# Kernel optimization log

Hardware: AMD Instinct MI355X
Metric: run time of the kernel (lower is better)

## Reference

```python
import jax, jax.numpy as jnp
import numpy as np

B, T, C = 2, 192, 512
H, D = 8, 64  # num_heads, head_dim; inner_dim = H*D = C


def setup_inputs() -> dict:
    key = jax.random.key(0)
    k1, k2, k3 = jax.random.split(key, 3)
    x = jax.random.normal(k1, (B, T, C), dtype=jnp.float32)
    W_in = jax.random.normal(k2, (C, 5 * H * D), dtype=jnp.float32) * 0.02
    b_in = jnp.zeros((5 * H * D,), dtype=jnp.float32)
    W_out = jax.random.normal(k3, (H * D, C), dtype=jnp.float32) * 0.02
    b_out = jnp.zeros((C,), dtype=jnp.float32)
    return {"x": x, "W_in": W_in, "b_in": b_in, "W_out": W_out, "b_out": b_out}


def _split_heads(t):
    # (B,T,H*D) -> (B,H,T,D)
    return t.reshape(B, T, H, D).transpose(0, 2, 1, 3)


def reference(x, W_in, b_in, W_out, b_out):
    scale = D ** -0.5
    proj = x @ W_in + b_in  # (B,T,5*H*D)
    q, k1, v1, k2, v2 = jnp.split(proj, 5, axis=-1)
    q = _split_heads(q) * scale
    k1 = _split_heads(k1)
    v1 = _split_heads(v1)
    k2 = _split_heads(k2)
    v2 = _split_heads(v2)
    # trilinear logits: <q_i, k1_j, k2_k> / sqrt(D), computed in fp32
    logits = jnp.einsum('bhid,bhjd,bhkd->bhijk', q, k1, k2,
                        preferred_element_type=jnp.float32)
    # softmax over the joint (j,k) axes
    attn = jax.nn.softmax(logits.reshape(B, H, T, T * T), axis=-1)
    attn = attn.reshape(B, H, T, T, T).astype(x.dtype)
    # out_i[d] = sum_{j,k} attn[i,j,k] * v1_j[d] * v2_k[d]
    out = jnp.einsum('bhijk,bhjd,bhkd->bhid', attn, v1, v2)
    y = out.transpose(0, 2, 1, 3).reshape(B, T, H * D)  # merge heads
    return y @ W_out + b_out
```

## Files before the change

kernel.cpp:

```cpp
#include <hip/hip_runtime.h>


typedef float  v4f __attribute__((ext_vector_type(4)));
typedef short  v8s __attribute__((ext_vector_type(8)));

__device__ __forceinline__ unsigned short f2bf(float f) {
  unsigned u = __float_as_uint(f);
  u += 0x7fffu + ((u >> 16) & 1u);
  return (unsigned short)(u >> 16);
}
__device__ __forceinline__ float bf2f(unsigned short b) {
  return __uint_as_float(((unsigned)b) << 16);
}

#if __has_builtin(__builtin_amdgcn_exp2f)
#define EXP2F(x) __builtin_amdgcn_exp2f(x)
#else
#define EXP2F(x) exp2f(x)
#endif

#define MFMA32(a, b, c) __builtin_amdgcn_mfma_f32_16x16x32_bf16((a), (b), (c), 0, 0, 0)

#define QSCALE 0.18033688011112042f


__global__ __launch_bounds__(256) void proj_kernel(
    const float* __restrict__ x, const float* __restrict__ Win,
    const float* __restrict__ bin, float* __restrict__ wsf,
    unsigned short* __restrict__ wsh) {
  __shared__ float xs[8 * 512];
  __shared__ float red[8 * 128];
  const int tid = threadIdx.x;
  const int r0 = blockIdx.x * 8;
  const int jj = tid & 127, half = tid >> 7;
  const int j = blockIdx.y * 128 + jj;

  const float4* xsrc = (const float4*)(x + r0 * 512);
  float4* xdst = (float4*)xs;
  for (int idx = tid; idx < 1024; idx += 256) xdst[idx] = xsrc[idx];
  __syncthreads();

  float acc[8];
#pragma unroll
  for (int r = 0; r < 8; ++r) acc[r] = 0.f;
  const float* wp = Win + (half * 256) * 2560 + j;
  const float* xp = xs + half * 256;
#pragma unroll 4
  for (int k = 0; k < 256; ++k) {
    const float w = wp[k * 2560];
#pragma unroll
    for (int r = 0; r < 8; ++r) acc[r] = fmaf(xp[r * 512 + k], w, acc[r]);
  }
  if (half) {
#pragma unroll
    for (int r = 0; r < 8; ++r) red[r * 128 + jj] = acc[r];
  }
  __syncthreads();
  if (!half) {
    const float bv = bin[j];
    const int which = j >> 9, cc = j & 511, h = cc >> 6, d = cc & 63;
#pragma unroll
    for (int r = 0; r < 8; ++r) {
      const int m = r0 + r;
      const int b = (m >= 192) ? 1 : 0;
      const int t = m - (b ? 192 : 0);
      const int bh = b * 8 + h;
      const float val = acc[r] + red[r * 128 + jj] + bv;
      const int rm = ((bh * 192 + t) << 6) + d;
      if (which == 0)      wsf[rm] = val * QSCALE;
      else if (which == 1) wsh[rm] = f2bf(val);
      else if (which == 2) wsh[393216 + ((bh << 6) + d) * 192 + t] = f2bf(val);
      else if (which == 3) wsh[196608 + rm] = f2bf(val);
      else                 wsf[196608 + rm] = val;
    }
  }
}

__global__ __launch_bounds__(256, 2) void attn_kernel(
    const float* __restrict__ wsf, const unsigned short* __restrict__ wsh,
    float* __restrict__ accp, float* __restrict__ Sp) {
  __shared__ unsigned short smem[64 * 200 + 4 * 16 * 40];
  unsigned short* V1s = smem;

  const int tid  = threadIdx.x;
  const int wv   = tid >> 6;
  const int lane = tid & 63;
  const int c    = lane & 15;
  const int quad = lane >> 4;

  const int bb = blockIdx.x;
  const int kb = bb & 3;
  const int it = (bb >> 2) % 12;
  const int bh = bb / 48;

  const unsigned short* k1g = wsh + bh * 192 * 64;
  const unsigned short* v1g = wsh + 393216 + bh * 64 * 192;
  const unsigned short* k2g = wsh + 196608 + bh * 192 * 64;
  const float*          v2g = wsf + 196608 + bh * 192 * 64;

  for (int idx = tid; idx < 1536; idx += 256) {
    const int r = idx / 24, c8 = (idx % 24) * 8;
    *(uint4*)(V1s + r * 200 + c8) = *(const uint4*)(v1g + r * 192 + c8);
  }

  v8s k1f[12][2];
#pragma unroll
  for (int jt = 0; jt < 12; ++jt) {
    const unsigned short* kp = k1g + ((jt * 16 + c) << 6) + (quad << 3);
    k1f[jt][0] = *(const v8s*)(kp);
    k1f[jt][1] = *(const v8s*)(kp + 32);
  }

  const float* qg = wsf + ((bh * 192 + it * 16 + c) << 6) + (quad << 3);
  float q0[8], q1[8];
  {
    v4f qa = *(const v4f*)(qg), qb = *(const v4f*)(qg + 4);
    v4f qc = *(const v4f*)(qg + 32), qd = *(const v4f*)(qg + 36);
#pragma unroll
    for (int e = 0; e < 4; ++e) {
      q0[e] = qa[e]; q0[4 + e] = qb[e];
      q1[e] = qc[e]; q1[4 + e] = qd[e];
    }
  }
  __syncthreads();

  unsigned short* Pch = smem + 12800 + wv * 640;
  const v4f z = {0.f, 0.f, 0.f, 0.f};
  v4f acc0 = z, acc1 = z, acc2 = z, acc3 = z;
  float S0 = 0.f, S1 = 0.f, S2 = 0.f, S3 = 0.f;

  const int kstart = kb * 48 + wv * 12;
  for (int s = 0; s < 12; ++s) {
    const int k = kstart + s;
    const unsigned short* k2r = k2g + (k << 6) + (quad << 3);
    union { uint4 u4; unsigned short us[8]; } kl, kh;
    kl.u4 = *(const uint4*)k2r;
    kh.u4 = *(const uint4*)(k2r + 32);
    const float* v2r = v2g + (k << 6) + c;
    const float v20 = v2r[0], v21 = v2r[16], v22 = v2r[32], v23 = v2r[48];

    union { v8s v; unsigned short us[8]; } af0, af1;
#pragma unroll
    for (int e = 0; e < 8; ++e) {
      af0.us[e] = f2bf(q0[e] * bf2f(kl.us[e]));
      af1.us[e] = f2bf(q1[e] * bf2f(kh.us[e]));
    }

    v4f o0 = z, o1 = z, o2 = z, o3 = z;
#pragma unroll
    for (int jp = 0; jp < 6; ++jp) {
#pragma unroll
      for (int jj2 = 0; jj2 < 2; ++jj2) {
        const int jt = jp * 2 + jj2;
        v4f Cf = MFMA32(af0.v, k1f[jt][0], z);
        Cf = MFMA32(af1.v, k1f[jt][1], Cf);
        unsigned short* wp2 = Pch + (quad << 2) * 40 + jj2 * 16 + c;
        const float p0 = EXP2F(Cf[0]), p1 = EXP2F(Cf[1]);
        const float p2 = EXP2F(Cf[2]), p3 = EXP2F(Cf[3]);
        S0 += p0; S1 += p1; S2 += p2; S3 += p3;
        wp2[0]   = (unsigned short)(__float_as_uint(p0) >> 16);
        wp2[40]  = (unsigned short)(__float_as_uint(p1) >> 16);
        wp2[80]  = (unsigned short)(__float_as_uint(p2) >> 16);
        wp2[120] = (unsigned short)(__float_as_uint(p3) >> 16);
      }
      const v8s ap = *(const v8s*)(Pch + c * 40 + (quad << 3));
      const int vcol = jp * 32 + (quad << 3);
      o0 = MFMA32(ap, *(const v8s*)(V1s + (c)      * 200 + vcol), o0);
      o1 = MFMA32(ap, *(const v8s*)(V1s + (c + 16) * 200 + vcol), o1);
      o2 = MFMA32(ap, *(const v8s*)(V1s + (c + 32) * 200 + vcol), o2);
      o3 = MFMA32(ap, *(const v8s*)(V1s + (c + 48) * 200 + vcol), o3);
    }
    acc0 += o0 * v20; acc1 += o1 * v21; acc2 += o2 * v22; acc3 += o3 * v23;
  }

  __syncthreads();
  float* redA = (float*)smem;
  float* redS = (float*)smem + 4096;

#pragma unroll
  for (int m2 = 1; m2 < 16; m2 <<= 1) {
    S0 += __shfl_xor(S0, m2, 16);
    S1 += __shfl_xor(S1, m2, 16);
    S2 += __shfl_xor(S2, m2, 16);
    S3 += __shfl_xor(S3, m2, 16);
  }
  if (c == 0) {
    float* rs = redS + wv * 16 + (quad << 2);
    rs[0] = S0; rs[1] = S1; rs[2] = S2; rs[3] = S3;
  }
#pragma unroll
  for (int r = 0; r < 4; ++r) {
    float* rr = redA + wv * 1024 + (((quad << 2) + r) << 6) + c;
    rr[0] = acc0[r]; rr[16] = acc1[r]; rr[32] = acc2[r]; rr[48] = acc3[r];
  }
  __syncthreads();

  const int pbase = (bh * 12 + it) * 4 + kb;
  float* ap_out = accp + pbase * 1024;
  for (int idx = tid; idx < 1024; idx += 256)
    ap_out[idx] = redA[idx] + redA[1024 + idx] + redA[2048 + idx] + redA[3072 + idx];
  if (tid < 16)
    Sp[pbase * 16 + tid] = redS[tid] + redS[16 + tid] + redS[32 + tid] + redS[48 + tid];
}

__global__ __launch_bounds__(256) void outp_kernel(
    const float* __restrict__ accp, const float* __restrict__ Sp,
    const float* __restrict__ Wout, const float* __restrict__ bout,
    float* __restrict__ y) {
  __shared__ float as[4 * 512];
  __shared__ float red[4 * 128];
  const int tid = threadIdx.x;
  const int r0 = blockIdx.x * 4;
  for (int idx = tid; idx < 2048; idx += 256) {
    const int r = idx >> 9, cc = idx & 511;
    const int m = r0 + r;
    const int b = (m >= 192) ? 1 : 0;
    const int t = m - (b ? 192 : 0);
    const int h = cc >> 6, d = cc & 63;
    const int bh = b * 8 + h, itl = t >> 4, i = t & 15;
    const int pb = (bh * 12 + itl) * 4;
    float a = 0.f, Sv = 0.f;
#pragma unroll
    for (int s2 = 0; s2 < 4; ++s2) {
      a  += accp[(pb + s2) * 1024 + (i << 6) + d];
      Sv += Sp[(pb + s2) * 16 + i];
    }
    as[idx] = a / Sv;
  }
  __syncthreads();

  const int jj = tid & 127, half = tid >> 7;
  const int j = blockIdx.y * 128 + jj;
  float acc[4];
#pragma unroll
  for (int r = 0; r < 4; ++r) acc[r] = 0.f;
  const float* wp = Wout + (half * 256) * 512 + j;
  const float* xp = as + half * 256;
#pragma unroll 4
  for (int k = 0; k < 256; ++k) {
    const float w = wp[k * 512];
#pragma unroll
    for (int r = 0; r < 4; ++r) acc[r] = fmaf(xp[r * 512 + k], w, acc[r]);
  }
  if (half) {
#pragma unroll
    for (int r = 0; r < 4; ++r) red[r * 128 + jj] = acc[r];
  }
  __syncthreads();
  if (!half) {
    const float bv = bout[j];
#pragma unroll
    for (int r = 0; r < 4; ++r)
      y[(r0 + r) * 512 + j] = acc[r] + red[r * 128 + jj] + bv;
  }
}

extern "C" void kernel_launch(void* const* d_in, const int* in_sizes, int n_in,
                              void* d_out, int out_size, void* d_ws, size_t ws_size,
                              hipStream_t stream) {
  const float* x    = (const float*)d_in[0];
  const float* Win  = (const float*)d_in[1];
  const float* bin  = (const float*)d_in[2];
  const float* Wout = (const float*)d_in[3];
  const float* bout = (const float*)d_in[4];

  float* wsf = (float*)d_ws;
  unsigned short* wsh = (unsigned short*)(wsf + 1191936);
  float* accp = wsf + 393216;
  float* Sp   = wsf + 1179648;

  proj_kernel<<<dim3(48, 20), 256, 0, stream>>>(x, Win, bin, wsf, wsh);
  attn_kernel<<<dim3(768), 256, 0, stream>>>(wsf, wsh, accp, Sp);
  outp_kernel<<<dim3(96, 4), 256, 0, stream>>>(accp, Sp, Wout, bout, (float*)d_out);
}
```

Baseline: 167.8 us.

## Move input and output projections to split-bf16 MFMA GEMMs with prefetching

Replaces the scalar fp32 FMA projection GEMMs with bf16 MFMA GEMMs. Each fp32 operand is split into a high and a low bf16 part, and three products are accumulated to keep near-fp32 accuracy. A prep kernel converts and transposes the weights and x every call, and a new norm kernel produces the split normalized attention output. The attention kernel now prefetches the next k2/v2 row and reads v2 from a re-laid-out vector-friendly layout. This adds two extra kernel launches and extra workspace traffic in exchange for using the matrix cores.

Measured after the change: 156.6 us. -6.7%, faster.

```diff
diff --git a/kernel.cpp b/kernel.cpp
--- a/kernel.cpp
+++ b/kernel.cpp
@@ -24,54 +24,124 @@
 #define QSCALE 0.18033688011112042f
 
 
-__global__ __launch_bounds__(256) void proj_kernel(
+#define XH_OFF   589824
+#define XL_OFF   786432
+#define WTH_OFF  983040
+#define WTL_OFF  2293760
+#define WOTH_OFF 3604480
+#define WOTL_OFF 3866624
+#define OH_OFF   4128768
+#define OL_OFF   4325376
+
+__global__ __launch_bounds__(256) void prep_kernel(
     const float* __restrict__ x, const float* __restrict__ Win,
-    const float* __restrict__ bin, float* __restrict__ wsf,
-    unsigned short* __restrict__ wsh) {
-  __shared__ float xs[8 * 512];
-  __shared__ float red[8 * 128];
-  const int tid = threadIdx.x;
-  const int r0 = blockIdx.x * 8;
-  const int jj = tid & 127, half = tid >> 7;
-  const int j = blockIdx.y * 128 + jj;
-
-  const float4* xsrc = (const float4*)(x + r0 * 512);
-  float4* xdst = (float4*)xs;
-  for (int idx = tid; idx < 1024; idx += 256) xdst[idx] = xsrc[idx];
-  __syncthreads();
-
-  float acc[8];
-#pragma unroll
-  for (int r = 0; r < 8; ++r) acc[r] = 0.f;
-  const float* wp = Win + (half * 256) * 2560 + j;
-  const float* xp = xs + half * 256;
-#pragma unroll 4
-  for (int k = 0; k < 256; ++k) {
-    const float w = wp[k * 2560];
-#pragma unroll
-    for (int r = 0; r < 8; ++r) acc[r] = fmaf(xp[r * 512 + k], w, acc[r]);
-  }
-  if (half) {
-#pragma unroll
-    for (int r = 0; r < 8; ++r) red[r * 128 + jj] = acc[r];
-  }
-  __syncthreads();
-  if (!half) {
-    const float bv = bin[j];
-    const int which = j >> 9, cc = j & 511, h = cc >> 6, d = cc & 63;
-#pragma unroll
-    for (int r = 0; r < 8; ++r) {
-      const int m = r0 + r;
-      const int b = (m >= 192) ? 1 : 0;
-      const int t = m - (b ? 192 : 0);
-      const int bh = b * 8 + h;
-      const float val = acc[r] + red[r * 128 + jj] + bv;
-      const int rm = ((bh * 192 + t) << 6) + d;
-      if (which == 0)      wsf[rm] = val * QSCALE;
-      else if (which == 1) wsh[rm] = f2bf(val);
-      else if (which == 2) wsh[393216 + ((bh << 6) + d) * 192 + t] = f2bf(val);
-      else if (which == 3) wsh[196608 + rm] = f2bf(val);
-      else                 wsf[196608 + rm] = val;
+    const float* __restrict__ Wout, unsigned short* __restrict__ wsh) {
+  const int bi = blockIdx.x, t = threadIdx.x;
+  if (bi < 768) {
+    const float* W; unsigned short *Th, *Tl; int R, n0, k0;
+    if (bi < 640) {
+      W = Win; Th = wsh + WTH_OFF; Tl = wsh + WTL_OFF; R = 2560;
+      n0 = (bi % 40) << 6; k0 = (bi / 40) << 5;
+    } else {
+      const int idx = bi - 640;
+      W = Wout; Th = wsh + WOTH_OFF; Tl = wsh + WOTL_OFF; R = 512;
+      n0 = (idx & 7) << 6; k0 = (idx >> 3) << 5;
+    }
+    const int n = n0 + (t & 63);
+    const int kg = k0 + (t >> 6) * 8;
+    float v[8];
+#pragma unroll
+    for (int j = 0; j < 8; ++j) v[j] = W[(kg + j) * R + n];
+    union { uint4 u; unsigned short us[8]; } ph, pl;
+#pragma unroll
+    for (int j = 0; j < 8; ++j) {
+      const unsigned short h = f2bf(v[j]);
+      ph.us[j] = h;
+      pl.us[j] = f2bf(v[j] - bf2f(h));
+    }
+    *(uint4*)(Th + n * 512 + kg) = ph.u;
+    *(uint4*)(Tl + n * 512 + kg) = pl.u;
+  } else {
+    const int flat = ((bi - 768) * 256 + t) * 8;
+    const v4f v0 = *(const v4f*)(x + flat);
+    const v4f v1 = *(const v4f*)(x + flat + 4);
+    union { uint4 u; unsigned short us[8]; } ph, pl;
+#pragma unroll
+    for (int j = 0; j < 4; ++j) {
+      unsigned short h = f2bf(v0[j]);
+      ph.us[j] = h; pl.us[j] = f2bf(v0[j] - bf2f(h));
+      h = f2bf(v1[j]);
+      ph.us[4 + j] = h; pl.us[4 + j] = f2bf(v1[j] - bf2f(h));
+    }
+    *(uint4*)(wsh + XH_OFF + flat) = ph.u;
+    *(uint4*)(wsh + XL_OFF + flat) = pl.u;
+  }
+}
+
+__global__ __launch_bounds__(64) void proj_kernel(
+    const unsigned short* __restrict__ wsh, const float* __restrict__ bin,
+    float* __restrict__ wsf, unsigned short* __restrict__ wshd) {
+  const int lane = threadIdx.x;
+  const int c = lane & 15, q = lane >> 4;
+  const int bm = blockIdx.x % 12, bn = blockIdx.x / 12;
+
+  const unsigned short* ah0 = wsh + XH_OFF + (bm * 32 + c) * 512 + (q << 3);
+  const unsigned short* ah1 = ah0 + 16 * 512;
+  const unsigned short* al0 = wsh + XL_OFF + (bm * 32 + c) * 512 + (q << 3);
+  const unsigned short* al1 = al0 + 16 * 512;
+  const unsigned short* bh0 = wsh + WTH_OFF + (bn * 32 + c) * 512 + (q << 3);
+  const unsigned short* bh1 = bh0 + 16 * 512;
+  const unsigned short* bl0 = wsh + WTL_OFF + (bn * 32 + c) * 512 + (q << 3);
+  const unsigned short* bl1 = bl0 + 16 * 512;
+
+  const v4f z = {0.f, 0.f, 0.f, 0.f};
+  v4f a00 = z, a01 = z, a10 = z, a11 = z;
+
+  v8s cAh0 = *(const v8s*)ah0, cAh1 = *(const v8s*)ah1;
+  v8s cAl0 = *(const v8s*)al0, cAl1 = *(const v8s*)al1;
+  v8s cBh0 = *(const v8s*)bh0, cBh1 = *(const v8s*)bh1;
+  v8s cBl0 = *(const v8s*)bl0, cBl1 = *(const v8s*)bl1;
+
+#pragma unroll 1
+  for (int ks = 0; ks < 16; ++ks) {
+    v8s nAh0, nAh1, nAl0, nAl1, nBh0, nBh1, nBl0, nBl1;
+    if (ks < 15) {
+      const int o = (ks + 1) * 32;
+      nAh0 = *(const v8s*)(ah0 + o); nAh1 = *(const v8s*)(ah1 + o);
+      nAl0 = *(const v8s*)(al0 + o); nAl1 = *(const v8s*)(al1 + o);
+      nBh0 = *(const v8s*)(bh0 + o); nBh1 = *(const v8s*)(bh1 + o);
+      nBl0 = *(const v8s*)(bl0 + o); nBl1 = *(const v8s*)(bl1 + o);
+    }
+    a00 = MFMA32(cAl0, cBh0, a00); a00 = MFMA32(cAh0, cBl0, a00); a00 = MFMA32(cAh0, cBh0, a00);
+    a01 = MFMA32(cAl0, cBh1, a01); a01 = MFMA32(cAh0, cBl1, a01); a01 = MFMA32(cAh0, cBh1, a01);
+    a10 = MFMA32(cAl1, cBh0, a10); a10 = MFMA32(cAh1, cBl0, a10); a10 = MFMA32(cAh1, cBh0, a10);
+    a11 = MFMA32(cAl1, cBh1, a11); a11 = MFMA32(cAh1, cBl1, a11); a11 = MFMA32(cAh1, cBh1, a11);
+    cAh0 = nAh0; cAh1 = nAh1; cAl0 = nAl0; cAl1 = nAl1;
+    cBh0 = nBh0; cBh1 = nBh1; cBl0 = nBl0; cBl1 = nBl1;
+  }
+
+  v4f accs[2][2] = {{a00, a01}, {a10, a11}};
+#pragma unroll
+  for (int mt = 0; mt < 2; ++mt) {
+#pragma unroll
+    for (int nt = 0; nt < 2; ++nt) {
+      const int n = bn * 32 + nt * 16 + c;
+      const int which = n >> 9, cc = n & 511, h = cc >> 6, d = cc & 63;
+      const float bv = bin[n];
+#pragma unroll
+      for (int r = 0; r < 4; ++r) {
+        const int m = bm * 32 + mt * 16 + (q << 2) + r;
+        const int b = (m >= 192) ? 1 : 0;
+        const int tt = m - (b ? 192 : 0);
+        const int bh = b * 8 + h;
+        const float val = accs[mt][nt][r] + bv;
+        const int rm = ((bh * 192 + tt) << 6) + d;
+        if (which == 0)      wsf[rm] = val * QSCALE;
+        else if (which == 1) wshd[rm] = f2bf(val);
+        else if (which == 2) wshd[393216 + ((bh << 6) + d) * 192 + tt] = f2bf(val);
+        else if (which == 3) wshd[196608 + rm] = f2bf(val);
+        else wsf[196608 + ((bh * 192 + tt) * 16 + (d & 15)) * 4 + (d >> 4)] = val;
+      }
     }
   }
 }
@@ -96,7 +166,7 @@
   const unsigned short* k1g = wsh + bh * 192 * 64;
   const unsigned short* v1g = wsh + 393216 + bh * 64 * 192;
   const unsigned short* k2g = wsh + 196608 + bh * 192 * 64;
-  const float*          v2g = wsf + 196608 + bh * 192 * 64;
+  const float*          v2g = wsf + 196608 + bh * 12288;
 
   for (int idx = tid; idx < 1536; idx += 256) {
     const int r = idx / 24, c8 = (idx % 24) * 8;
@@ -130,14 +200,19 @@
   float S0 = 0.f, S1 = 0.f, S2 = 0.f, S3 = 0.f;
 
   const int kstart = kb * 48 + wv * 12;
+  union { uint4 u4; unsigned short us[8]; } kl, kh, nkl, nkh;
+  kl.u4 = *(const uint4*)(k2g + (kstart << 6) + (quad << 3));
+  kh.u4 = *(const uint4*)(k2g + (kstart << 6) + (quad << 3) + 32);
+  v4f v2 = *(const v4f*)(v2g + ((kstart * 16 + c) << 2));
+
   for (int s = 0; s < 12; ++s) {
-    const int k = kstart + s;
-    const unsigned short* k2r = k2g + (k << 6) + (quad << 3);
-    union { uint4 u4; unsigned short us[8]; } kl, kh;
-    kl.u4 = *(const uint4*)k2r;
-    kh.u4 = *(const uint4*)(k2r + 32);
-    const float* v2r = v2g + (k << 6) + c;
-    const float v20 = v2r[0], v21 = v2r[16], v22 = v2r[32], v23 = v2r[48];
+    v4f nv2;
+    if (s < 11) {
+      const int k2o = ((kstart + s + 1) << 6) + (quad << 3);
+      nkl.u4 = *(const uint4*)(k2g + k2o);
+      nkh.u4 = *(const uint4*)(k2g + k2o + 32);
+      nv2 = *(const v4f*)(v2g + (((kstart + s + 1) * 16 + c) << 2));
+    }
 
     union { v8s v; unsigned short us[8]; } af0, af1;
 #pragma unroll
@@ -170,7 +245,8 @@
       o2 = MFMA32(ap, *(const v8s*)(V1s + (c + 32) * 200 + vcol), o2);
       o3 = MFMA32(ap, *(const v8s*)(V1s + (c + 48) * 200 + vcol), o3);
     }
-    acc0 += o0 * v20; acc1 += o1 * v21; acc2 += o2 * v22; acc3 += o3 * v23;
+    acc0 += o0 * v2[0]; acc1 += o1 * v2[1]; acc2 += o2 * v2[2]; acc3 += o3 * v2[3];
+    kl = nkl; kh = nkh; v2 = nv2;
   }
 
   __syncthreads();
@@ -203,55 +279,95 @@
     Sp[pbase * 16 + tid] = redS[tid] + redS[16 + tid] + redS[32 + tid] + redS[48 + tid];
 }
 
-__global__ __launch_bounds__(256) void outp_kernel(
+__global__ __launch_bounds__(256) void norm_kernel(
     const float* __restrict__ accp, const float* __restrict__ Sp,
-    const float* __restrict__ Wout, const float* __restrict__ bout,
+    unsigned short* __restrict__ wsh) {
+  const int flat = blockIdx.x * 2048 + threadIdx.x * 8;
+  const int m = flat >> 9, cc = flat & 511;
+  const int b = (m >= 192) ? 1 : 0;
+  const int tt = m - (b ? 192 : 0);
+  const int h = cc >> 6, d0 = cc & 63;
+  const int bh = b * 8 + h, it = tt >> 4, i = tt & 15;
+  const int pb = (bh * 12 + it) * 4;
+  const float* ap = accp + pb * 1024 + (i << 6) + d0;
+  v4f a0 = *(const v4f*)(ap), a1 = *(const v4f*)(ap + 4);
+  float Sv = Sp[pb * 16 + i];
+#pragma unroll
+  for (int kb = 1; kb < 4; ++kb) {
+    a0 += *(const v4f*)(ap + kb * 1024);
+    a1 += *(const v4f*)(ap + kb * 1024 + 4);
+    Sv += Sp[(pb + kb) * 16 + i];
+  }
+  const float inv = 1.0f / Sv;
+  union { uint4 u; unsigned short us[8]; } ph, pl;
+#pragma unroll
+  for (int j = 0; j < 4; ++j) {
+    float v = a0[j] * inv;
+    unsigned short hh = f2bf(v);
+    ph.us[j] = hh; pl.us[j] = f2bf(v - bf2f(hh));
+    v = a1[j] * inv;
+    hh = f2bf(v);
+    ph.us[4 + j] = hh; pl.us[4 + j] = f2bf(v - bf2f(hh));
+  }
+  *(uint4*)(wsh + OH_OFF + flat) = ph.u;
+  *(uint4*)(wsh + OL_OFF + flat) = pl.u;
+}
+
+__global__ __launch_bounds__(64) void outp_kernel(
+    const unsigned short* __restrict__ wsh, const float* __restrict__ bout,
     float* __restrict__ y) {
-  __shared__ float as[4 * 512];
-  __shared__ float red[4 * 128];
-  const int tid = threadIdx.x;
-  const int r0 = blockIdx.x * 4;
-  for (int idx = tid; idx < 2048; idx += 256) {
-    const int r = idx >> 9, cc = idx & 511;
-    const int m = r0 + r;
-    const int b = (m >= 192) ? 1 : 0;
-    const int t = m - (b ? 192 : 0);
-    const int h = cc >> 6, d = cc & 63;
-    const int bh = b * 8 + h, itl = t >> 4, i = t & 15;
-    const int pb = (bh * 12 + itl) * 4;
-    float a = 0.f, Sv = 0.f;
-#pragma unroll
-    for (int s2 = 0; s2 < 4; ++s2) {
-      a  += accp[(pb + s2) * 1024 + (i << 6) + d];
-      Sv += Sp[(pb + s2) * 16 + i];
-    }
-    as[idx] = a / Sv;
-  }
-  __syncthreads();
-
-  const int jj = tid & 127, half = tid >> 7;
-  const int j = blockIdx.y * 128 + jj;
-  float acc[4];
-#pragma unroll
-  for (int r = 0; r < 4; ++r) acc[r] = 0.f;
-  const float* wp = Wout + (half * 256) * 512 + j;
-  const float* xp = as + half * 256;
-#pragma unroll 4
-  for (int k = 0; k < 256; ++k) {
-    const float w = wp[k * 512];
-#pragma unroll
-    for (int r = 0; r < 4; ++r) acc[r] = fmaf(xp[r * 512 + k], w, acc[r]);
-  }
-  if (half) {
-#pragma unroll
-    for (int r = 0; r < 4; ++r) red[r * 128 + jj] = acc[r];
-  }
-  __syncthreads();
-  if (!half) {
-    const float bv = bout[j];
-#pragma unroll
-    for (int r = 0; r < 4; ++r)
-      y[(r0 + r) * 512 + j] = acc[r] + red[r * 128 + jj] + bv;
+  const int lane = threadIdx.x;
+  const int c = lane & 15, q = lane >> 4;
+  const int bm = blockIdx.x % 12, bn = blockIdx.x / 12;
+
+  const unsigned short* ah0 = wsh + OH_OFF + (bm * 32 + c) * 512 + (q << 3);
+  const unsigned short* ah1 = ah0 + 16 * 512;
+  const unsigned short* al0 = wsh + OL_OFF + (bm * 32 + c) * 512 + (q << 3);
+  const unsigned short* al1 = al0 + 16 * 512;
+  const unsigned short* bh0 = wsh + WOTH_OFF + (bn * 32 + c) * 512 + (q << 3);
+  const unsigned short* bh1 = bh0 + 16 * 512;
+  const unsigned short* bl0 = wsh + WOTL_OFF + (bn * 32 + c) * 512 + (q << 3);
+  const unsigned short* bl1 = bl0 + 16 * 512;
+
+  const v4f z = {0.f, 0.f, 0.f, 0.f};
+  v4f a00 = z, a01 = z, a10 = z, a11 = z;
+
+  v8s cAh0 = *(const v8s*)ah0, cAh1 = *(const v8s*)ah1;
+  v8s cAl0 = *(const v8s*)al0, cAl1 = *(const v8s*)al1;
+  v8s cBh0 = *(const v8s*)bh0, cBh1 = *(const v8s*)bh1;
+  v8s cBl0 = *(const v8s*)bl0, cBl1 = *(const v8s*)bl1;
+
+#pragma unroll 1
+  for (int ks = 0; ks < 16; ++ks) {
+    v8s nAh0, nAh1, nAl0, nAl1, nBh0, nBh1, nBl0, nBl1;
+    if (ks < 15) {
+      const int o = (ks + 1) * 32;
+      nAh0 = *(const v8s*)(ah0 + o); nAh1 = *(const v8s*)(ah1 + o);
+      nAl0 = *(const v8s*)(al0 + o); nAl1 = *(const v8s*)(al1 + o);
+      nBh0 = *(const v8s*)(bh0 + o); nBh1 = *(const v8s*)(bh1 + o);
+      nBl0 = *(const v8s*)(bl0 + o); nBl1 = *(const v8s*)(bl1 + o);
+    }
+    a00 = MFMA32(cAl0, cBh0, a00); a00 = MFMA32(cAh0, cBl0, a00); a00 = MFMA32(cAh0, cBh0, a00);
+    a01 = MFMA32(cAl0, cBh1, a01); a01 = MFMA32(cAh0, cBl1, a01); a01 = MFMA32(cAh0, cBh1, a01);
+    a10 = MFMA32(cAl1, cBh0, a10); a10 = MFMA32(cAh1, cBl0, a10); a10 = MFMA32(cAh1, cBh0, a10);
+    a11 = MFMA32(cAl1, cBh1, a11); a11 = MFMA32(cAh1, cBl1, a11); a11 = MFMA32(cAh1, cBh1, a11);
+    cAh0 = nAh0; cAh1 = nAh1; cAl0 = nAl0; cAl1 = nAl1;
+    cBh0 = nBh0; cBh1 = nBh1; cBl0 = nBl0; cBl1 = nBl1;
+  }
+
+  v4f accs[2][2] = {{a00, a01}, {a10, a11}};
+#pragma unroll
+  for (int mt = 0; mt < 2; ++mt) {
+#pragma unroll
+    for (int nt = 0; nt < 2; ++nt) {
+      const int n = bn * 32 + nt * 16 + c;
+      const float bv = bout[n];
+#pragma unroll
+      for (int r = 0; r < 4; ++r) {
+        const int m = bm * 32 + mt * 16 + (q << 2) + r;
+        y[m * 512 + n] = accs[mt][nt][r] + bv;
+      }
+    }
   }
 }
 
@@ -269,7 +385,9 @@
   float* accp = wsf + 393216;
   float* Sp   = wsf + 1179648;
 
-  proj_kernel<<<dim3(48, 20), 256, 0, stream>>>(x, Win, bin, wsf, wsh);
+  prep_kernel<<<dim3(864), 256, 0, stream>>>(x, Win, Wout, wsh);
+  proj_kernel<<<dim3(960), 64, 0, stream>>>(wsh, bin, wsf, wsh);
   attn_kernel<<<dim3(768), 256, 0, stream>>>(wsf, wsh, accp, Sp);
-  outp_kernel<<<dim3(96, 4), 256, 0, stream>>>(accp, Sp, Wout, bout, (float*)d_out);
-}
+  norm_kernel<<<dim3(96), 256, 0, stream>>>(accp, Sp, wsh);
+  outp_kernel<<<dim3(192), 64, 0, stream>>>(wsh, bout, (float*)d_out);
+}
```
